# Optimization experiments

Hardware: AMD Instinct MI355X
Metric: run time of the kernel (lower is better)

Reference implementation:

```python
import jax, jax.numpy as jnp
import numpy as np

D = 256          # config.entity_dim
DQ = 256         # query feature dim
G = 512          # number of neighbor groups (len(num_neighbors))
PER = 128
N = G * PER      # total candidate entities
CH = [256, 512, 512, 256]  # TCN channel list [D, 2D, 2D, D]
K = 3            # TCN kernel size
HID = 512        # policy net hidden dim


def _p(key, shape):
    return jax.random.normal(key, shape, dtype=jnp.float32) * 0.02


def setup_inputs() -> dict:
    key = jax.random.key(0)
    ks = jax.random.split(key, 32)
    inp = {}
    inp["NEs"] = jax.random.normal(ks[0], (N, D), dtype=jnp.float32)
    inp["nodes"] = jax.random.normal(ks[1], (G, D), dtype=jnp.float32)
    inp["query"] = jax.random.normal(ks[2], (G, DQ), dtype=jnp.float32)
    inp["num_neighbors"] = jnp.full((G,), PER, dtype=jnp.int32)
    inp["action_index"] = jax.random.randint(ks[3], (G,), 0, PER, dtype=jnp.int32)
    # action encoder (linear + relu)
    inp["Wa"] = _p(ks[4], (D, D))
    inp["ba"] = jnp.zeros((D,), jnp.float32)
    # TCN: 4 dilated causal conv levels, 1x1 downsample where channels change
    cin, i = D, 5
    for l, cout in enumerate(CH):
        inp[f"Wc{l}"] = _p(ks[i], (cout, cin, K)); i += 1
        inp[f"bc{l}"] = jnp.zeros((cout,), jnp.float32)
        if cout != cin:
            inp[f"Wd{l}"] = _p(ks[i], (cout, cin)); i += 1
        cin = cout
    # policy net MLP over [state_HS_per_candidate ; hat]
    inp["Wp1"] = _p(ks[i], (DQ + 2 * D + D, HID))
    inp["bp1"] = jnp.zeros((HID,), jnp.float32)
    inp["Wp2"] = _p(ks[i + 1], (HID, 1))
    inp["bp2"] = jnp.zeros((1,), jnp.float32)
    return inp


def _causal_conv(x, w, b, dil):
    # x: [1, C_in, L], w: [C_out, C_in, K] -> causal (left-padded) dilated conv
    k = w.shape[-1]
    y = jax.lax.conv_general_dilated(
        x, w, window_strides=(1,), padding=[((k - 1) * dil, 0)],
        rhs_dilation=(dil,), dimension_numbers=("NCH", "OIH", "NCH"))
    return y + b[None, :, None]


def _tcn(x, params):
    for (w, b, wd), dil in zip(params, (1, 2, 4, 8)):
        y = jax.nn.relu(_causal_conv(x, w, b, dil))
        res = x if wd is None else jnp.einsum("oi,bil->bol", wd, x)
        x = jax.nn.relu(y + res)
    return x


def reference(NEs, nodes, query, num_neighbors, action_index, Wa, ba,
              Wc0, bc0, Wc1, bc1, Wd1, Wc2, bc2, Wc3, bc3, Wd3,
              Wp1, bp1, Wp2, bp2):
    counts = np.asarray(num_neighbors)            # static ragged segment sizes
    g = counts.shape[0]
    seg = jnp.asarray(np.repeat(np.arange(g), counts))
    offsets = np.concatenate([[0], np.cumsum(counts)[:-1]])
    act = np.asarray(action_index)

    hats = jax.nn.relu(NEs @ Wa + ba)                         # [N, D]
    # _Max per group = column-wise max over each ragged segment
    HAts = jax.ops.segment_max(hats, seg, num_segments=g)     # [G, D]
    # chosen-action row per group (last group contributes no hat/node in the loop)
    hats_sel = hats[jnp.asarray(offsets[: g - 1] + act[: g - 1])]  # [G-1, D]

    # state_seq rows: (node_i, HAt_i, hat_i) for i < G-1, then nodes[-1]
    body = jnp.stack([nodes[: g - 1], HAts[: g - 1], hats_sel], axis=1)
    body = body.reshape(3 * (g - 1), -1)
    state_seq = jnp.concatenate([body, nodes[-1:]], axis=0)   # [L, D], L = 3(G-1)+1

    x = state_seq.T[None]                                     # [1, D, L]
    x = _tcn(x, [(Wc0, bc0, None), (Wc1, bc1, Wd1), (Wc2, bc2, None), (Wc3, bc3, Wd3)])
    hs = x[0].T[np.arange(g) * 3]                             # gather node positions -> [G, D]

    state_HS = jnp.concatenate([query, hs, HAts], axis=1)     # [G, DQ + 2D]
    rep = jnp.repeat(state_HS, jnp.asarray(counts), axis=0)   # [N, DQ + 2D]
    h = jax.nn.relu(jnp.concatenate([rep, hats], axis=1) @ Wp1 + bp1)
    Qsa = h @ Wp2 + bp2                                       # [N, 1]
    return Qsa
```

## Files before the change

kernel.cpp:

```cpp
#include <hip/hip_runtime.h>
#include <hip/hip_bf16.h>

#define D 256
#define G 512
#define PER 128
#define NROW (G*PER)
#define LSEQ 1534
#define LP 1536
#define HID 512

typedef __hip_bfloat16 bf16;
typedef __attribute__((ext_vector_type(8))) short bf16x8;
typedef __attribute__((ext_vector_type(4))) float f32x4;


__global__ __launch_bounds__(256) void k_zeroH(float4* __restrict__ p) {
  p[blockIdx.x * 256 + threadIdx.x] = make_float4(0.f, 0.f, 0.f, 0.f);
}

__global__ void k_waprep(const float* __restrict__ Wa,
                         bf16* __restrict__ WAhi, bf16* __restrict__ WAlo) {
  int id = blockIdx.x * 256 + threadIdx.x;
  int k = id >> 8, n = id & 255;
  float v = Wa[(size_t)k * D + n];
  bf16 h = __float2bfloat16(v);
  float hf = __bfloat162float(h);
  bf16 l = __float2bfloat16(v - hf);
  int dst = (n >> 7) * 32768
          + (((((n >> 4) & 7) * 8 + (k >> 5)) * 64 + ((k >> 3) & 3) * 16 + (n & 15)) * 8)
          + (k & 7);
  WAhi[dst] = h;
  WAlo[dst] = l;
}

__global__ __launch_bounds__(256) void k_hats_mfma(
    const float* __restrict__ NEs, const bf16* __restrict__ WAhi,
    const bf16* __restrict__ WAlo, const float* __restrict__ ba,
    bf16* __restrict__ hats, float* __restrict__ HAts) {
  __shared__ __align__(16) unsigned short bs[32768];
  __shared__ float wsmax[4][128];

  const int tid = threadIdx.x;
  const int wave = tid >> 6, lane = tid & 63;
  const int ln = lane & 15, quad = lane >> 4;
  const int row0 = blockIdx.x * 64;
  const int g = row0 >> 7;

  bf16x8 afH[8], afL[8];
  {
    const float4* ap = (const float4*)(NEs + (size_t)(row0 + wave*16 + ln) * D);
    #pragma unroll
    for (int kt = 0; kt < 8; ++kt) {
      float4 x0 = ap[kt*8 + quad*2];
      float4 x1 = ap[kt*8 + quad*2 + 1];
      float xv[8] = {x0.x, x0.y, x0.z, x0.w, x1.x, x1.y, x1.z, x1.w};
      bf16x8 hv, lv;
      #pragma unroll
      for (int e = 0; e < 8; ++e) {
        bf16 h = __float2bfloat16(xv[e]);
        bf16 l = __float2bfloat16(xv[e] - __bfloat162float(h));
        hv[e] = *(short*)&h;
        lv[e] = *(short*)&l;
      }
      afH[kt] = hv;
      afL[kt] = lv;
    }
  }

  float* bsf = (float*)bs;

  for (int chunk = 0; chunk < 2; ++chunk) {
    f32x4 acc[8];
    #pragma unroll
    for (int nt = 0; nt < 8; ++nt) acc[nt] = (f32x4){0.f, 0.f, 0.f, 0.f};

    __syncthreads();
    {
      const uint4* src = (const uint4*)(WAhi + (size_t)chunk * 32768);
      uint4* dst = (uint4*)bs;
      #pragma unroll
      for (int r = 0; r < 16; ++r) dst[r*256 + tid] = src[r*256 + tid];
    }
    __syncthreads();
    #pragma unroll
    for (int nt = 0; nt < 8; ++nt)
      #pragma unroll
      for (int kt = 0; kt < 8; ++kt) {
        const bf16x8 bfr = *(const bf16x8*)&bs[((nt*8 + kt)*64 + lane)*8];
        acc[nt] = __builtin_amdgcn_mfma_f32_16x16x32_bf16(afH[kt], bfr, acc[nt], 0, 0, 0);
        acc[nt] = __builtin_amdgcn_mfma_f32_16x16x32_bf16(afL[kt], bfr, acc[nt], 0, 0, 0);
      }

    __syncthreads();
    {
      const uint4* src = (const uint4*)(WAlo + (size_t)chunk * 32768);
      uint4* dst = (uint4*)bs;
      #pragma unroll
      for (int r = 0; r < 16; ++r) dst[r*256 + tid] = src[r*256 + tid];
    }
    __syncthreads();
    #pragma unroll
    for (int nt = 0; nt < 8; ++nt)
      #pragma unroll
      for (int kt = 0; kt < 8; ++kt) {
        const bf16x8 bfr = *(const bf16x8*)&bs[((nt*8 + kt)*64 + lane)*8];
        acc[nt] = __builtin_amdgcn_mfma_f32_16x16x32_bf16(afH[kt], bfr, acc[nt], 0, 0, 0);
      }

    __syncthreads();
    #pragma unroll
    for (int nt = 0; nt < 8; ++nt) {
      const float bv = ba[chunk*128 + nt*16 + ln];
      float m = 0.f;
      #pragma unroll
      for (int reg = 0; reg < 4; ++reg) {
        float h = acc[nt][reg] + bv;
        h = h > 0.f ? h : 0.f;
        bsf[(wave*16 + quad*4 + reg)*140 + nt*16 + ln] = h;
        m = fmaxf(m, h);
      }
      m = fmaxf(m, __shfl_xor(m, 16, 64));
      m = fmaxf(m, __shfl_xor(m, 32, 64));
      if (quad == 0) wsmax[wave][nt*16 + ln] = m;
    }
    __syncthreads();
    {
      const int row = tid >> 2, q4 = tid & 3;
      const float* rp = &bsf[row*140 + q4*32];
      bf16* gp = hats + (size_t)(row0 + row) * D + chunk*128 + q4*32;
      #pragma unroll
      for (int s = 0; s < 4; ++s) {
        float4 v0 = *(const float4*)&rp[s*8];
        float4 v1 = *(const float4*)&rp[s*8 + 4];
        float vv[8] = {v0.x, v0.y, v0.z, v0.w, v1.x, v1.y, v1.z, v1.w};
        bf16x8 pk;
        #pragma unroll
        for (int e = 0; e < 8; ++e) {
          bf16 b = __float2bfloat16(vv[e]);
          pk[e] = *(short*)&b;
        }
        *(bf16x8*)(gp + s*8) = pk;
      }
    }
    if (tid < 128) {
      float m = fmaxf(fmaxf(wsmax[0][tid], wsmax[1][tid]),
                      fmaxf(wsmax[2][tid], wsmax[3][tid]));
      atomicMax((unsigned int*)&HAts[(size_t)g*D + chunk*128 + tid],
                __float_as_uint(m));
    }
  }
}

__global__ void k_wconv(const float* __restrict__ Wp1, bf16* __restrict__ WBt) {
  int id = blockIdx.x * 256 + threadIdx.x;
  int k = id >> 9, n = id & 511;
  float v = Wp1[(size_t)(768 + k) * HID + n];
  int dst = (n >> 7) * 32768
          + (((((n >> 4) & 7) * 8 + (k >> 5)) * 64 + ((k >> 3) & 3) * 16 + (n & 15)) * 8)
          + (k & 7);
  WBt[dst] = __float2bfloat16(v);
}

__global__ void k_wp1prep(const float* __restrict__ Wp1,
                          bf16* __restrict__ Bhi, bf16* __restrict__ Blo) {
  int id = blockIdx.x * 256 + threadIdx.x;
  int k = id >> 9, n = id & 511;
  float v = Wp1[(size_t)k * HID + n];
  bf16 h = __float2bfloat16(v);
  bf16 l = __float2bfloat16(v - __bfloat162float(h));
  int kc = k >> 8, kr = k & 255;
  int nc = n >> 7, nr = n & 127;
  int dst = (nc*3 + kc) * 32768
          + ((((nr >> 4) * 8 + (kr >> 5)) * 64 + ((kr >> 3) & 3) * 16 + (nr & 15)) * 8)
          + (kr & 7);
  Bhi[dst] = h;
  Blo[dst] = l;
}

__global__ void k_sprep(const float* __restrict__ query,
                        const float* __restrict__ HAts,
                        const float* __restrict__ xfin,
                        bf16* __restrict__ Shi, bf16* __restrict__ Slo) {
  int m = blockIdx.x * 256 + threadIdx.x;
  int g = blockIdx.y;
  float v;
  if (m < 256)      v = query[(size_t)g*D + m];
  else if (m < 512) v = xfin[(size_t)(m - 256)*LP + 3*g];
  else              v = HAts[(size_t)g*D + (m - 512)];
  bf16 h = __float2bfloat16(v);
  bf16 l = __float2bfloat16(v - __bfloat162float(h));
  Shi[(size_t)g*768 + m] = h;
  Slo[(size_t)g*768 + m] = l;
}

__global__ __launch_bounds__(256) void k_gterm_mfma(
    const bf16* __restrict__ Shi, const bf16* __restrict__ Slo,
    const bf16* __restrict__ WB1hi, const bf16* __restrict__ WB1lo,
    const float* __restrict__ bp1, float* __restrict__ Gterm) {
  __shared__ __align__(16) unsigned short bs[32768];

  const int tid = threadIdx.x;
  const int wave = tid >> 6, lane = tid & 63;
  const int ln = lane & 15, quad = lane >> 4;
  const int nc = blockIdx.x;
  const int row0 = blockIdx.y * 64;

  f32x4 acc[8];
  #pragma unroll
  for (int nt = 0; nt < 8; ++nt) acc[nt] = (f32x4){0.f, 0.f, 0.f, 0.f};

  const uint4* ahp = (const uint4*)(Shi + (size_t)(row0 + wave*16 + ln) * 768);
  const uint4* alp = (const uint4*)(Slo + (size_t)(row0 + wave*16 + ln) * 768);

  for (int kc = 0; kc < 3; ++kc) {
    bf16x8 afH[8], afL[8];
    #pragma unroll
    for (int kt = 0; kt < 8; ++kt) {
      uint4 th = ahp[kc*32 + kt*4 + quad];
      uint4 tl = alp[kc*32 + kt*4 + quad];
      afH[kt] = *(const bf16x8*)&th;
      afL[kt] = *(const bf16x8*)&tl;
    }

    __syncthreads();
    {
      const uint4* src = (const uint4*)(WB1hi + (size_t)(nc*3 + kc) * 32768);
      uint4* dst = (uint4*)bs;
      #pragma unroll
      for (int r = 0; r < 16; ++r) dst[r*256 + tid] = src[r*256 + tid];
    }
    __syncthreads();
    #pragma unroll
    for (int nt = 0; nt < 8; ++nt)
      #pragma unroll
      for (int kt = 0; kt < 8; ++kt) {
        const bf16x8 bfr = *(const bf16x8*)&bs[((nt*8 + kt)*64 + lane)*8];
        acc[nt] = __builtin_amdgcn_mfma_f32_16x16x32_bf16(afH[kt], bfr, acc[nt], 0, 0, 0);
        acc[nt] = __builtin_amdgcn_mfma_f32_16x16x32_bf16(afL[kt], bfr, acc[nt], 0, 0, 0);
      }

    __syncthreads();
    {
      const uint4* src = (const uint4*)(WB1lo + (size_t)(nc*3 + kc) * 32768);
      uint4* dst = (uint4*)bs;
      #pragma unroll
      for (int r = 0; r < 16; ++r) dst[r*256 + tid] = src[r*256 + tid];
    }
    __syncthreads();
    #pragma unroll
    for (int nt = 0; nt < 8; ++nt)
      #pragma unroll
      for (int kt = 0; kt < 8; ++kt) {
        const bf16x8 bfr = *(const bf16x8*)&bs[((nt*8 + kt)*64 + lane)*8];
        acc[nt] = __builtin_amdgcn_mfma_f32_16x16x32_bf16(afH[kt], bfr, acc[nt], 0, 0, 0);
      }
  }

  #pragma unroll
  for (int nt = 0; nt < 8; ++nt) {
    const int col = nc*128 + nt*16 + ln;
    const float bv = bp1[col];
    #pragma unroll
    for (int reg = 0; reg < 4; ++reg)
      Gterm[(size_t)(row0 + wave*16 + quad*4 + reg) * HID + col] = acc[nt][reg] + bv;
  }
}

__global__ void k_build_x0(const float* __restrict__ nodes,
                           const float* __restrict__ HAts,
                           const bf16* __restrict__ hats,
                           const int* __restrict__ act,
                           float* __restrict__ x0) {
  int t = blockIdx.x * 256 + threadIdx.x;
  int c = blockIdx.y;
  if (t >= LSEQ) return;
  float v;
  if (t == LSEQ - 1) {
    v = nodes[(size_t)(G-1)*D + c];
  } else {
    int r = t / 3, m = t - 3*r;
    if (m == 0)      v = nodes[(size_t)r*D + c];
    else if (m == 1) v = HAts[(size_t)r*D + c];
    else             v = __bfloat162float(hats[(size_t)(r*PER + act[r])*D + c]);
  }
  x0[(size_t)c*LP + t] = v;
}

template<int DIL, int CPB, bool HASWD>
__global__ __launch_bounds__(256) void k_tcn4(
    const float* __restrict__ xin,
    const float* __restrict__ W,
    const float* __restrict__ Wd,
    float* __restrict__ ybuf,
    float* __restrict__ rbuf,
    int Cin) {
  __shared__ __align__(16) float xs[32][80];
  __shared__ __align__(16) float wst[3][32][68];
  __shared__ __align__(16) float wds[HASWD ? 32 : 1][HASWD ? 68 : 4];

  const int tid = threadIdx.x;
  const int tt = tid & 15;
  const int cc = tid >> 4;
  const int t0 = blockIdx.x * 64;
  const int o0 = blockIdx.y * 64;
  const int Cout = gridDim.y << 6;

  float acc[4][4], res[4][4];
  #pragma unroll
  for (int it = 0; it < 4; ++it)
    #pragma unroll
    for (int ic = 0; ic < 4; ++ic) { acc[it][ic] = 0.f; res[it][ic] = 0.f; }

  for (int c = 0; c < CPB; ++c) {
    const int i0 = (blockIdx.z * CPB + c) * 32;
    __syncthreads();
    for (int idx = tid; idx < 32*20; idx += 256) {
      int r = idx / 20, j4 = idx - r*20;
      int tp = t0 - 16 + j4*4;
      float4 v;
      if (tp >= 0) v = *(const float4*)&xin[(size_t)(i0 + r)*LP + tp];
      else         v = make_float4(0.f, 0.f, 0.f, 0.f);
      *(float4*)&xs[r][j4*4] = v;
    }
    for (int idx = tid; idx < 64*32; idx += 256) {
      int o = idx >> 5, i = idx & 31;
      const float* wp = &W[((size_t)(o0 + o)*Cin + i0 + i)*3];
      wst[0][i][o] = wp[0];
      wst[1][i][o] = wp[1];
      wst[2][i][o] = wp[2];
      if constexpr (HASWD) wds[i][o] = Wd[(size_t)(o0 + o)*Cin + i0 + i];
    }
    __syncthreads();

    const int base = 16 + tt*4;
    #pragma unroll 2
    for (int i = 0; i < 32; ++i) {
      float4 xv0, xv1, xv2;
      if constexpr (DIL == 1) {
        float4 A = *(const float4*)&xs[i][base - 4];
        float4 B = *(const float4*)&xs[i][base];
        xv0 = make_float4(A.z, A.w, B.x, B.y);
        xv1 = make_float4(A.w, B.x, B.y, B.z);
        xv2 = B;
      } else if constexpr (DIL == 2) {
        float4 A = *(const float4*)&xs[i][base - 4];
        float4 B = *(const float4*)&xs[i][base];
        xv0 = A;
        xv1 = make_float4(A.z, A.w, B.x, B.y);
        xv2 = B;
      } else {
        xv0 = *(const float4*)&xs[i][base - 2*DIL];
        xv1 = *(const float4*)&xs[i][base - DIL];
        xv2 = *(const float4*)&xs[i][base];
      }
      float4 w0 = *(const float4*)&wst[0][i][cc*4];
      float4 w1 = *(const float4*)&wst[1][i][cc*4];
      float4 w2 = *(const float4*)&wst[2][i][cc*4];
      #pragma unroll
      for (int it = 0; it < 4; ++it) {
        float x0 = ((const float*)&xv0)[it];
        float x1 = ((const float*)&xv1)[it];
        float x2 = ((const float*)&xv2)[it];
        #pragma unroll
        for (int ic = 0; ic < 4; ++ic) {
          float a = acc[it][ic];
          a = fmaf(x0, ((const float*)&w0)[ic], a);
          a = fmaf(x1, ((const float*)&w1)[ic], a);
          a = fmaf(x2, ((const float*)&w2)[ic], a);
          acc[it][ic] = a;
        }
      }
      if constexpr (HASWD) {
        float4 wd4 = *(const float4*)&wds[i][cc*4];
        #pragma unroll
        for (int it = 0; it < 4; ++it) {
          float x2 = ((const float*)&xv2)[it];
          #pragma unroll
          for (int ic = 0; ic < 4; ++ic)
            res[it][ic] = fmaf(x2, ((const float*)&wd4)[ic], res[it][ic]);
        }
      }
    }
  }

  const int t = t0 + tt*4;
  #pragma unroll
  for (int ic = 0; ic < 4; ++ic) {
    const int ch = o0 + cc*4 + ic;
    const size_t off = ((size_t)blockIdx.z * Cout + ch) * LP + t;
    float4 v = make_float4(acc[0][ic], acc[1][ic], acc[2][ic], acc[3][ic]);
    *(float4*)&ybuf[off] = v;
    if constexpr (HASWD) {
      float4 rv = make_float4(res[0][ic], res[1][ic], res[2][ic], res[3][ic]);
      *(float4*)&rbuf[off] = rv;
    }
  }
}

template<int NZ, bool HASWD>
__global__ __launch_bounds__(384) void k_tcn_red(
    const float* __restrict__ ybuf, const float* __restrict__ rbuf,
    const float* __restrict__ xin, const float* __restrict__ b,
    float* __restrict__ xout) {
  const int ch = blockIdx.x;
  const int Cout = gridDim.x;
  const int t = threadIdx.x * 4;
  const size_t stride = (size_t)Cout * LP;
  const size_t base = (size_t)ch * LP + t;

  float4 y = *(const float4*)&ybuf[base];
  #pragma unroll
  for (int z = 1; z < NZ; ++z) {
    float4 u = *(const float4*)&ybuf[base + z*stride];
    y.x += u.x; y.y += u.y; y.z += u.z; y.w += u.w;
  }
  const float bv = b[ch];
  y.x = fmaxf(y.x + bv, 0.f); y.y = fmaxf(y.y + bv, 0.f);
  y.z = fmaxf(y.z + bv, 0.f); y.w = fmaxf(y.w + bv, 0.f);

  float4 r;
  if constexpr (HASWD) {
    r = *(const float4*)&rbuf[base];
    #pragma unroll
    for (int z = 1; z < NZ; ++z) {
      float4 u = *(const float4*)&rbuf[base + z*stride];
      r.x += u.x; r.y += u.y; r.z += u.z; r.w += u.w;
    }
  } else {
    r = *(const float4*)&xin[base];
  }
  float4 v;
  v.x = fmaxf(y.x + r.x, 0.f); v.y = fmaxf(y.y + r.y, 0.f);
  v.z = fmaxf(y.z + r.z, 0.f); v.w = fmaxf(y.w + r.w, 0.f);
  *(float4*)&xout[base] = v;
}

__global__ __launch_bounds__(256) void k_final_mfma(
    const bf16* __restrict__ hats, const bf16* __restrict__ WBt,
    const float* __restrict__ Gterm, const float* __restrict__ Wp2,
    const float* __restrict__ bp2, float* __restrict__ out) {
  __shared__ __align__(16) unsigned short bs[32768];
  __shared__ float gs[512];
  __shared__ float w2s[512];

  const int tid = threadIdx.x;
  const int wave = tid >> 6, lane = tid & 63;
  const int ln = lane & 15, quad = lane >> 4;
  const int row0 = blockIdx.x * 64;
  const int g = row0 >> 7;

  gs[tid]        = Gterm[(size_t)g*HID + tid];
  gs[tid + 256]  = Gterm[(size_t)g*HID + tid + 256];
  w2s[tid]       = Wp2[tid];
  w2s[tid + 256] = Wp2[tid + 256];

  bf16x8 afrag[8];
  {
    const uint4* ap = (const uint4*)(hats + (size_t)(row0 + wave*16 + ln) * D);
    #pragma unroll
    for (int kt = 0; kt < 8; ++kt) {
      uint4 t = ap[kt*4 + quad];
      afrag[kt] = *(const bf16x8*)&t;
    }
  }

  float osum[4] = {0.f, 0.f, 0.f, 0.f};

  for (int chunk = 0; chunk < 4; ++chunk) {
    __syncthreads();
    const uint4* src = (const uint4*)(WBt + (size_t)chunk * 32768);
    uint4* dst = (uint4*)bs;
    #pragma unroll
    for (int r = 0; r < 16; ++r) dst[r*256 + tid] = src[r*256 + tid];
    __syncthreads();

    #pragma unroll
    for (int nt = 0; nt < 8; ++nt) {
      f32x4 acc = {0.f, 0.f, 0.f, 0.f};
      #pragma unroll
      for (int kt = 0; kt < 8; ++kt) {
        const bf16x8 bfr = *(const bf16x8*)&bs[((nt*8 + kt)*64 + lane)*8];
        acc = __builtin_amdgcn_mfma_f32_16x16x32_bf16(afrag[kt], bfr, acc, 0, 0, 0);
      }
      int n = chunk*128 + nt*16 + ln;
      float gv = gs[n], wv = w2s[n];
      #pragma unroll
      for (int reg = 0; reg < 4; ++reg) {
        float h = acc[reg] + gv;
        h = h > 0.f ? h : 0.f;
        osum[reg] = fmaf(h, wv, osum[reg]);
      }
    }
  }

  #pragma unroll
  for (int reg = 0; reg < 4; ++reg) {
    float v = osum[reg];
    v += __shfl_xor(v, 1, 64);
    v += __shfl_xor(v, 2, 64);
    v += __shfl_xor(v, 4, 64);
    v += __shfl_xor(v, 8, 64);
    osum[reg] = v;
  }
  if (ln == 0) {
    float b2 = bp2[0];
    #pragma unroll
    for (int reg = 0; reg < 4; ++reg)
      out[row0 + wave*16 + quad*4 + reg] = osum[reg] + b2;
  }
}

extern "C" void kernel_launch(void* const* d_in, const int* in_sizes, int n_in,
                              void* d_out, int out_size, void* d_ws, size_t ws_size,
                              hipStream_t stream) {
  (void)in_sizes; (void)n_in; (void)out_size; (void)ws_size;
  const float* NEs   = (const float*)d_in[0];
  const float* nodes = (const float*)d_in[1];
  const float* query = (const float*)d_in[2];
  const int*   act   = (const int*)d_in[4];
  const float* Wa    = (const float*)d_in[5];
  const float* ba    = (const float*)d_in[6];
  const float* Wc0   = (const float*)d_in[7];
  const float* bc0   = (const float*)d_in[8];
  const float* Wc1   = (const float*)d_in[9];
  const float* bc1   = (const float*)d_in[10];
  const float* Wd1   = (const float*)d_in[11];
  const float* Wc2   = (const float*)d_in[12];
  const float* bc2   = (const float*)d_in[13];
  const float* Wc3   = (const float*)d_in[14];
  const float* bc3   = (const float*)d_in[15];
  const float* Wd3   = (const float*)d_in[16];
  const float* Wp1   = (const float*)d_in[17];
  const float* bp1   = (const float*)d_in[18];
  const float* Wp2   = (const float*)d_in[19];
  const float* bp2   = (const float*)d_in[20];
  float* out = (float*)d_out;

  char* ws = (char*)d_ws;
  bf16*  hats  = (bf16*)ws;  ws += (size_t)NROW * D * sizeof(bf16);
  float* HAts  = (float*)ws; ws += (size_t)G * D * sizeof(float);
  float* xa    = (float*)ws; ws += (size_t)512 * LP * sizeof(float);
  float* xb    = (float*)ws; ws += (size_t)512 * LP * sizeof(float);
  float* Gterm = (float*)ws; ws += (size_t)G * HID * sizeof(float);
  bf16*  WBt   = (bf16*)ws;  ws += (size_t)D * HID * sizeof(bf16);
  bf16*  WAhi  = (bf16*)ws;  ws += (size_t)D * D * sizeof(bf16);
  bf16*  WAlo  = (bf16*)ws;  ws += (size_t)D * D * sizeof(bf16);
  bf16*  WB1hi = (bf16*)ws;  ws += (size_t)768 * HID * sizeof(bf16);
  bf16*  WB1lo = (bf16*)ws;  ws += (size_t)768 * HID * sizeof(bf16);
  bf16*  Shi   = (bf16*)ws;  ws += (size_t)G * 768 * sizeof(bf16);
  bf16*  Slo   = (bf16*)ws;  ws += (size_t)G * 768 * sizeof(bf16);
  float* P0 = (float*)ws; ws += (size_t)2048 * LP * sizeof(float);
  float* P1 = (float*)ws; ws += (size_t)2048 * LP * sizeof(float);

  k_zeroH<<<G*D/1024, 256, 0, stream>>>((float4*)HAts);
  k_waprep<<<256, 256, 0, stream>>>(Wa, WAhi, WAlo);
  k_hats_mfma<<<NROW/64, 256, 0, stream>>>(NEs, WAhi, WAlo, ba, hats, HAts);
  k_wconv<<<512, 256, 0, stream>>>(Wp1, WBt);
  k_wp1prep<<<1536, 256, 0, stream>>>(Wp1, WB1hi, WB1lo);
  k_build_x0<<<dim3(6, 256), 256, 0, stream>>>(nodes, HAts, hats, act, xa);

  k_tcn4<1, 1, false><<<dim3(24, 4, 8), 256, 0, stream>>>(xa, Wc0, nullptr, P0, nullptr, 256);
  k_tcn_red<8, false><<<256, 384, 0, stream>>>(P0, nullptr, xa, bc0, xb);
  k_tcn4<2, 2, true ><<<dim3(24, 8, 4), 256, 0, stream>>>(xb, Wc1, Wd1, P0, P1, 256);
  k_tcn_red<4, true ><<<512, 384, 0, stream>>>(P0, P1, xb, bc1, xa);
  k_tcn4<4, 4, false><<<dim3(24, 8, 4), 256, 0, stream>>>(xa, Wc2, nullptr, P0, nullptr, 512);
  k_tcn_red<4, false><<<512, 384, 0, stream>>>(P0, nullptr, xa, bc2, xb);
  k_tcn4<8, 2, true ><<<dim3(24, 4, 8), 256, 0, stream>>>(xb, Wc3, Wd3, P0, P1, 512);
  k_tcn_red<8, true ><<<256, 384, 0, stream>>>(P0, P1, xb, bc3, xa);

  k_sprep<<<dim3(3, G), 256, 0, stream>>>(query, HAts, xa, Shi, Slo);
  k_gterm_mfma<<<dim3(4, 8), 256, 0, stream>>>(Shi, Slo, WB1hi, WB1lo, bp1, Gterm);
  k_final_mfma<<<NROW/64, 256, 0, stream>>>(hats, WBt, Gterm, Wp2, bp2, out);
}
```

Measured before the change: 373.0 us.

## Fuse weight-prep kernels and give each group one 512-thread block

Merges the three weight-preparation kernels into one launch and removes the HAts zeroing kernel. The hats and final MFMA kernels now use one 512-thread block per group covering all 128 rows, so the segment max is done entirely in shared memory and written directly instead of through atomicMax. This cuts launch count, atomic traffic and the number of times weight tiles are reloaded from global memory. The trade-off is fewer, larger blocks, which may lower occupancy and raise register pressure at launch_bounds 512.

```diff
diff --git a/kernel.cpp b/kernel.cpp
--- a/kernel.cpp
+++ b/kernel.cpp
@@ -14,37 +14,58 @@
 typedef __attribute__((ext_vector_type(4))) float f32x4;
 
 
-__global__ __launch_bounds__(256) void k_zeroH(float4* __restrict__ p) {
-  p[blockIdx.x * 256 + threadIdx.x] = make_float4(0.f, 0.f, 0.f, 0.f);
-}
-
-__global__ void k_waprep(const float* __restrict__ Wa,
-                         bf16* __restrict__ WAhi, bf16* __restrict__ WAlo) {
-  int id = blockIdx.x * 256 + threadIdx.x;
-  int k = id >> 8, n = id & 255;
-  float v = Wa[(size_t)k * D + n];
-  bf16 h = __float2bfloat16(v);
-  float hf = __bfloat162float(h);
-  bf16 l = __float2bfloat16(v - hf);
-  int dst = (n >> 7) * 32768
-          + (((((n >> 4) & 7) * 8 + (k >> 5)) * 64 + ((k >> 3) & 3) * 16 + (n & 15)) * 8)
-          + (k & 7);
-  WAhi[dst] = h;
-  WAlo[dst] = l;
-}
-
-__global__ __launch_bounds__(256) void k_hats_mfma(
+__global__ __launch_bounds__(256) void k_prep(
+    const float* __restrict__ Wa, bf16* __restrict__ WAhi, bf16* __restrict__ WAlo,
+    const float* __restrict__ Wp1, bf16* __restrict__ WBt,
+    bf16* __restrict__ WB1hi, bf16* __restrict__ WB1lo) {
+  const int b = blockIdx.x, tid = threadIdx.x;
+  if (b < 256) {
+    int id = b * 256 + tid;
+    int k = id >> 8, n = id & 255;
+    float v = Wa[(size_t)k * D + n];
+    bf16 h = __float2bfloat16(v);
+    bf16 l = __float2bfloat16(v - __bfloat162float(h));
+    int dst = (n >> 7) * 32768
+            + (((((n >> 4) & 7) * 8 + (k >> 5)) * 64 + ((k >> 3) & 3) * 16 + (n & 15)) * 8)
+            + (k & 7);
+    WAhi[dst] = h;
+    WAlo[dst] = l;
+  } else if (b < 768) {
+    int id = (b - 256) * 256 + tid;
+    int k = id >> 9, n = id & 511;
+    float v = Wp1[(size_t)(768 + k) * HID + n];
+    int dst = (n >> 7) * 32768
+            + (((((n >> 4) & 7) * 8 + (k >> 5)) * 64 + ((k >> 3) & 3) * 16 + (n & 15)) * 8)
+            + (k & 7);
+    WBt[dst] = __float2bfloat16(v);
+  } else {
+    int id = (b - 768) * 256 + tid;
+    int k = id >> 9, n = id & 511;
+    float v = Wp1[(size_t)k * HID + n];
+    bf16 h = __float2bfloat16(v);
+    bf16 l = __float2bfloat16(v - __bfloat162float(h));
+    int kc = k >> 8, kr = k & 255;
+    int nc = n >> 7, nr = n & 127;
+    int dst = (nc*3 + kc) * 32768
+            + ((((nr >> 4) * 8 + (kr >> 5)) * 64 + ((kr >> 3) & 3) * 16 + (nr & 15)) * 8)
+            + (kr & 7);
+    WB1hi[dst] = h;
+    WB1lo[dst] = l;
+  }
+}
+
+__global__ __launch_bounds__(512) void k_hats_mfma(
     const float* __restrict__ NEs, const bf16* __restrict__ WAhi,
     const bf16* __restrict__ WAlo, const float* __restrict__ ba,
     bf16* __restrict__ hats, float* __restrict__ HAts) {
-  __shared__ __align__(16) unsigned short bs[32768];
-  __shared__ float wsmax[4][128];
+  __shared__ __align__(16) unsigned short bs[36864];
+  __shared__ float wsmax[8][128];
 
   const int tid = threadIdx.x;
   const int wave = tid >> 6, lane = tid & 63;
   const int ln = lane & 15, quad = lane >> 4;
-  const int row0 = blockIdx.x * 64;
-  const int g = row0 >> 7;
+  const int row0 = blockIdx.x * 128;
+  const int g = blockIdx.x;
 
   bf16x8 afH[8], afL[8];
   {
@@ -79,7 +100,7 @@
       const uint4* src = (const uint4*)(WAhi + (size_t)chunk * 32768);
       uint4* dst = (uint4*)bs;
       #pragma unroll
-      for (int r = 0; r < 16; ++r) dst[r*256 + tid] = src[r*256 + tid];
+      for (int r = 0; r < 8; ++r) dst[r*512 + tid] = src[r*512 + tid];
     }
     __syncthreads();
     #pragma unroll
@@ -96,7 +117,7 @@
       const uint4* src = (const uint4*)(WAlo + (size_t)chunk * 32768);
       uint4* dst = (uint4*)bs;
       #pragma unroll
-      for (int r = 0; r < 16; ++r) dst[r*256 + tid] = src[r*256 + tid];
+      for (int r = 0; r < 8; ++r) dst[r*512 + tid] = src[r*512 + tid];
     }
     __syncthreads();
     #pragma unroll
@@ -143,38 +164,12 @@
       }
     }
     if (tid < 128) {
-      float m = fmaxf(fmaxf(wsmax[0][tid], wsmax[1][tid]),
-                      fmaxf(wsmax[2][tid], wsmax[3][tid]));
-      atomicMax((unsigned int*)&HAts[(size_t)g*D + chunk*128 + tid],
-                __float_as_uint(m));
-    }
-  }
-}
-
-__global__ void k_wconv(const float* __restrict__ Wp1, bf16* __restrict__ WBt) {
-  int id = blockIdx.x * 256 + threadIdx.x;
-  int k = id >> 9, n = id & 511;
-  float v = Wp1[(size_t)(768 + k) * HID + n];
-  int dst = (n >> 7) * 32768
-          + (((((n >> 4) & 7) * 8 + (k >> 5)) * 64 + ((k >> 3) & 3) * 16 + (n & 15)) * 8)
-          + (k & 7);
-  WBt[dst] = __float2bfloat16(v);
-}
-
-__global__ void k_wp1prep(const float* __restrict__ Wp1,
-                          bf16* __restrict__ Bhi, bf16* __restrict__ Blo) {
-  int id = blockIdx.x * 256 + threadIdx.x;
-  int k = id >> 9, n = id & 511;
-  float v = Wp1[(size_t)k * HID + n];
-  bf16 h = __float2bfloat16(v);
-  bf16 l = __float2bfloat16(v - __bfloat162float(h));
-  int kc = k >> 8, kr = k & 255;
-  int nc = n >> 7, nr = n & 127;
-  int dst = (nc*3 + kc) * 32768
-          + ((((nr >> 4) * 8 + (kr >> 5)) * 64 + ((kr >> 3) & 3) * 16 + (nr & 15)) * 8)
-          + (kr & 7);
-  Bhi[dst] = h;
-  Blo[dst] = l;
+      float m = wsmax[0][tid];
+      #pragma unroll
+      for (int w = 1; w < 8; ++w) m = fmaxf(m, wsmax[w][tid]);
+      HAts[(size_t)g*D + chunk*128 + tid] = m;
+    }
+  }
 }
 
 __global__ void k_sprep(const float* __restrict__ query,
@@ -435,7 +430,7 @@
   *(float4*)&xout[base] = v;
 }
 
-__global__ __launch_bounds__(256) void k_final_mfma(
+__global__ __launch_bounds__(512) void k_final_mfma(
     const bf16* __restrict__ hats, const bf16* __restrict__ WBt,
     const float* __restrict__ Gterm, const float* __restrict__ Wp2,
     const float* __restrict__ bp2, float* __restrict__ out) {
@@ -446,13 +441,11 @@
   const int tid = threadIdx.x;
   const int wave = tid >> 6, lane = tid & 63;
   const int ln = lane & 15, quad = lane >> 4;
-  const int row0 = blockIdx.x * 64;
-  const int g = row0 >> 7;
-
-  gs[tid]        = Gterm[(size_t)g*HID + tid];
-  gs[tid + 256]  = Gterm[(size_t)g*HID + tid + 256];
-  w2s[tid]       = Wp2[tid];
-  w2s[tid + 256] = Wp2[tid + 256];
+  const int row0 = blockIdx.x * 128;
+  const int g = blockIdx.x;
+
+  gs[tid]  = Gterm[(size_t)g*HID + tid];
+  w2s[tid] = Wp2[tid];
 
   bf16x8 afrag[8];
   {
@@ -471,7 +464,7 @@
     const uint4* src = (const uint4*)(WBt + (size_t)chunk * 32768);
     uint4* dst = (uint4*)bs;
     #pragma unroll
-    for (int r = 0; r < 16; ++r) dst[r*256 + tid] = src[r*256 + tid];
+    for (int r = 0; r < 8; ++r) dst[r*512 + tid] = src[r*512 + tid];
     __syncthreads();
 
     #pragma unroll
@@ -552,11 +545,8 @@
   float* P0 = (float*)ws; ws += (size_t)2048 * LP * sizeof(float);
   float* P1 = (float*)ws; ws += (size_t)2048 * LP * sizeof(float);
 
-  k_zeroH<<<G*D/1024, 256, 0, stream>>>((float4*)HAts);
-  k_waprep<<<256, 256, 0, stream>>>(Wa, WAhi, WAlo);
-  k_hats_mfma<<<NROW/64, 256, 0, stream>>>(NEs, WAhi, WAlo, ba, hats, HAts);
-  k_wconv<<<512, 256, 0, stream>>>(Wp1, WBt);
-  k_wp1prep<<<1536, 256, 0, stream>>>(Wp1, WB1hi, WB1lo);
+  k_prep<<<2304, 256, 0, stream>>>(Wa, WAhi, WAlo, Wp1, WBt, WB1hi, WB1lo);
+  k_hats_mfma<<<G, 512, 0, stream>>>(NEs, WAhi, WAlo, ba, hats, HAts);
   k_build_x0<<<dim3(6, 256), 256, 0, stream>>>(nodes, HAts, hats, act, xa);
 
   k_tcn4<1, 1, false><<<dim3(24, 4, 8), 256, 0, stream>>>(xa, Wc0, nullptr, P0, nullptr, 256);
@@ -570,5 +560,5 @@
 
   k_sprep<<<dim3(3, G), 256, 0, stream>>>(query, HAts, xa, Shi, Slo);
   k_gterm_mfma<<<dim3(4, 8), 256, 0, stream>>>(Shi, Slo, WB1hi, WB1lo, bp1, Gterm);
-  k_final_mfma<<<NROW/64, 256, 0, stream>>>(hats, WBt, Gterm, Wp2, bp2, out);
-}
+  k_final_mfma<<<G, 512, 0, stream>>>(hats, WBt, Gterm, Wp2, bp2, out);
+}
```

Result: faster. 355.5 us (-4.7%).
